# Optimization experiments

Hardware: AMD Instinct MI355X
Metric: run time of the kernel (lower is better)

Reference implementation:

```python
import jax, jax.numpy as jnp
import numpy as np

NUM_FEATURES = 512
NUM_HID = 16
NUM_CLASSES = 40


def _glorot(key, shape):
    lim = float(np.sqrt(6.0 / (shape[0] + shape[1])))
    return jax.random.uniform(key, shape, jnp.float32, -lim, lim)


def setup_inputs() -> dict:
    key = jax.random.key(0)
    k1, k2, k3, k4 = jax.random.split(key, 4)
    N, E = 100000, 3200000
    x = jax.random.normal(k1, (N, NUM_FEATURES), jnp.float32)
    edge_index = jax.random.randint(k2, (2, E), 0, N, jnp.int64)
    W1 = _glorot(k3, (NUM_FEATURES, NUM_HID))
    b1 = jnp.zeros((NUM_HID,), jnp.float32)
    W2 = _glorot(k4, (NUM_HID, NUM_CLASSES))
    b2 = jnp.zeros((NUM_CLASSES,), jnp.float32)
    return {"x": x, "edge_index": edge_index, "num_nodes": N,
            "W1": W1, "b1": b1, "W2": W2, "b2": b2}


def gcn_conv(x, src, dst, norm, W, b, num_nodes):
    # linear transform first (PyG GCNConv), then normalized scatter-add
    h = x @ W                                    # [N, out]
    msg = h[src] * norm[:, None]                 # [E+N, out]
    agg = jax.ops.segment_sum(msg, dst, num_segments=num_nodes)
    return agg + b


def reference(x, edge_index, num_nodes, W1, b1, W2, b2):
    # add self-loops and compute symmetric normalization deg^-1/2 A_hat deg^-1/2
    loops = jnp.arange(num_nodes, dtype=edge_index.dtype)
    src = jnp.concatenate([edge_index[0], loops])
    dst = jnp.concatenate([edge_index[1], loops])
    ones = jnp.ones(src.shape, x.dtype)
    deg = jax.ops.segment_sum(ones, dst, num_segments=num_nodes)
    dinv = jnp.where(deg > 0, deg ** -0.5, 0.0)
    norm = dinv[src] * dinv[dst]

    h = jax.nn.relu(gcn_conv(x, src, dst, norm, W1, b1, num_nodes))
    # dropout omitted: inference mode (training=False)
    h = gcn_conv(h, src, dst, norm, W2, b2, num_nodes)
    out = jax.nn.softmax(h, axis=1)
    return (out, h)
```

## Files before the change

kernel.cpp:

```cpp
#include <hip/hip_runtime.h>
#include <math.h>

#define F 512
#define H 16
#define C 40
#define BW 128
#define BSH 7
#define NB_MAX 1024
#define CHUNK 4096
#define SEGS 8
#define SRC_BITS 17
#define SRC_MASK 0x1FFFF
#define SORT_CAP 8192

__global__ __launch_bounds__(256) void k_hist2(const int* __restrict__ dst,
                                               int* __restrict__ M, int E, int NB) {
    __shared__ int hist[NB_MAX];
    int c = blockIdx.x, t = threadIdx.x;
    for (int b = t; b < NB; b += 256) hist[b] = 0;
    __syncthreads();
    int i0 = c * CHUNK, end = min(i0 + CHUNK, E);
    for (int i = i0 + t; i < end; i += 256)
        atomicAdd(&hist[dst[i] >> BSH], 1);
    __syncthreads();
    for (int b = t; b < NB; b += 256) M[(size_t)c * NB + b] = hist[b];
}

__global__ __launch_bounds__(256) void k_csA(const int* __restrict__ M, int* __restrict__ P,
                                             int NB, int NCH, int SEGLEN) {
    int t = blockIdx.x * 256 + threadIdx.x;
    if (t >= SEGS * NB) return;
    int s = t / NB, b = t - s * NB;
    int c0 = s * SEGLEN, c1 = min(c0 + SEGLEN, NCH);
    int sum = 0;
    for (int c = c0; c < c1; c++) sum += M[(size_t)c * NB + b];
    P[s * NB + b] = sum;
}

__global__ void k_csBscan(int* __restrict__ P, int* __restrict__ brow,
                          int* __restrict__ rowptr, int NB, int N, int E) {
    __shared__ int sh[1024];
    int t = threadIdx.x;
    int run = 0;
    if (t < NB) {
        #pragma unroll
        for (int s = 0; s < SEGS; s++) {
            int v = P[s * NB + t];
            P[s * NB + t] = run;
            run += v;
        }
    }
    sh[t] = run;
    __syncthreads();
    for (int off = 1; off < 1024; off <<= 1) {
        int add = (t >= off) ? sh[t - off] : 0;
        __syncthreads();
        sh[t] += add;
        __syncthreads();
    }
    if (t < NB) brow[t] = sh[t] - run;
    if (t == 0) { brow[NB] = E; rowptr[N] = E; }
}

__global__ __launch_bounds__(256) void k_csC(int* __restrict__ M, const int* __restrict__ P,
                                             const int* __restrict__ brow,
                                             int NB, int NCH, int SEGLEN) {
    int t = blockIdx.x * 256 + threadIdx.x;
    if (t >= SEGS * NB) return;
    int s = t / NB, b = t - s * NB;
    int c0 = s * SEGLEN, c1 = min(c0 + SEGLEN, NCH);
    int run = P[s * NB + b] + brow[b];
    for (int c = c0; c < c1; c++) {
        int v = M[(size_t)c * NB + b];
        M[(size_t)c * NB + b] = run;
        run += v;
    }
}

__global__ __launch_bounds__(256) void k_bscatter3(const int* __restrict__ src,
                                                   const int* __restrict__ dst,
                                                   const int* __restrict__ M,
                                                   int* __restrict__ ebuf, int E, int NB) {
    __shared__ int gbase[NB_MAX];
    __shared__ int pos[NB_MAX];
    __shared__ int cur[NB_MAX];
    __shared__ int tsum[256];
    __shared__ int paddr[CHUNK];
    __shared__ int pdata[CHUNK];
    int c = blockIdx.x, t = threadIdx.x;
    for (int b = t; b < NB; b += 256) {
        gbase[b] = M[(size_t)c * NB + b];
        cur[b] = 0;
    }
    __syncthreads();
    int i0 = c * CHUNK, end = min(i0 + CHUNK, E);
    for (int i = i0 + t; i < end; i += 256)
        atomicAdd(&cur[dst[i] >> BSH], 1);
    __syncthreads();
    int b0 = t * 4;
    int v0 = (b0 + 0 < NB) ? cur[b0 + 0] : 0;
    int v1 = (b0 + 1 < NB) ? cur[b0 + 1] : 0;
    int v2 = (b0 + 2 < NB) ? cur[b0 + 2] : 0;
    int v3 = (b0 + 3 < NB) ? cur[b0 + 3] : 0;
    int loc1 = v0, loc2 = v0 + v1, loc3 = v0 + v1 + v2;
    int s = loc3 + v3;
    tsum[t] = s;
    __syncthreads();
    for (int off = 1; off < 256; off <<= 1) {
        int v = (t >= off) ? tsum[t - off] : 0;
        __syncthreads();
        tsum[t] += v;
        __syncthreads();
    }
    int excl = tsum[t] - s;
    if (b0 + 0 < NB) { int p = excl;        pos[b0 + 0] = p; cur[b0 + 0] = p; }
    if (b0 + 1 < NB) { int p = excl + loc1; pos[b0 + 1] = p; cur[b0 + 1] = p; }
    if (b0 + 2 < NB) { int p = excl + loc2; pos[b0 + 2] = p; cur[b0 + 2] = p; }
    if (b0 + 3 < NB) { int p = excl + loc3; pos[b0 + 3] = p; cur[b0 + 3] = p; }
    __syncthreads();
    for (int i = i0 + t; i < end; i += 256) {
        int d = dst[i], sv = src[i];
        int b = d >> BSH;
        int r = atomicAdd(&cur[b], 1);
        paddr[r] = gbase[b] + (r - pos[b]);
        pdata[r] = ((d & (BW - 1)) << SRC_BITS) | sv;
    }
    __syncthreads();
    int n = end - i0;
    for (int i = t; i < n; i += 256)
        ebuf[paddr[i]] = pdata[i];
}

__global__ __launch_bounds__(256) void k_sortb(int* __restrict__ ebuf,
                                               const int* __restrict__ brow,
                                               int* __restrict__ rowptr,
                                               float* __restrict__ dinv, int N) {
    __shared__ int buf[SORT_CAP];
    __shared__ int hist[BW];
    __shared__ int off[BW];
    __shared__ int cur[BW];
    int b = blockIdx.x;
    int beg = brow[b], end = brow[b + 1];
    int len = end - beg;
    if (len > SORT_CAP) len = SORT_CAP;
    int tid = threadIdx.x;
    if (tid < BW) hist[tid] = 0;
    for (int i = tid; i < len; i += 256) buf[i] = ebuf[beg + i];
    __syncthreads();
    for (int i = tid; i < len; i += 256)
        atomicAdd(&hist[buf[i] >> SRC_BITS], 1);
    __syncthreads();
    if (tid < BW) off[tid] = hist[tid];
    __syncthreads();
    for (int d = 1; d < BW; d <<= 1) {
        int v = (tid < BW && tid >= d) ? off[tid - d] : 0;
        __syncthreads();
        if (tid < BW) off[tid] += v;
        __syncthreads();
    }
    if (tid < BW) {
        int excl = off[tid] - hist[tid];
        int n = b * BW + tid;
        if (n < N) {
            rowptr[n] = beg + excl;
            dinv[n] = rsqrtf((float)(hist[tid] + 1));
        }
        cur[tid] = excl;
    }
    __syncthreads();
    for (int i = tid; i < len; i += 256) {
        int w = buf[i];
        int r = atomicAdd(&cur[w >> SRC_BITS], 1);
        ebuf[beg + r] = w & SRC_MASK;
    }
}

#define KT 64
#define GST 68
__global__ __launch_bounds__(64) void k_gemm1(const float* __restrict__ x,
                                              const float* __restrict__ W1,
                                              const float* __restrict__ dinv,
                                              float* __restrict__ h0s, int N) {
    __shared__ float xs[64 * GST];
    int t = threadIdx.x;
    int n0 = blockIdx.x * 64;
    float acc[H];
    #pragma unroll
    for (int j = 0; j < H; j++) acc[j] = 0.f;
    for (int kt = 0; kt < F; kt += KT) {
        __syncthreads();
        #pragma unroll
        for (int p = 0; p < 16; p++) {
            int idx = t + (p << 6);
            int r = idx >> 4, c4 = idx & 15;
            int v = n0 + r; if (v >= N) v = N - 1;
            float4 val = *(const float4*)(x + (size_t)v * F + kt + (c4 << 2));
            *(float4*)&xs[r * GST + (c4 << 2)] = val;
        }
        __syncthreads();
        #pragma unroll
        for (int k4 = 0; k4 < 16; k4++) {
            float4 xv = *(const float4*)&xs[t * GST + (k4 << 2)];
            const float* w = W1 + (size_t)(kt + (k4 << 2)) * H;
            #pragma unroll
            for (int j = 0; j < H; j++) acc[j] = fmaf(xv.x, w[j], acc[j]);
            #pragma unroll
            for (int j = 0; j < H; j++) acc[j] = fmaf(xv.y, w[H + j], acc[j]);
            #pragma unroll
            for (int j = 0; j < H; j++) acc[j] = fmaf(xv.z, w[2 * H + j], acc[j]);
            #pragma unroll
            for (int j = 0; j < H; j++) acc[j] = fmaf(xv.w, w[3 * H + j], acc[j]);
        }
    }
    int v = n0 + t;
    if (v >= N) return;
    float dv = dinv[v];
    float4* o4 = (float4*)(h0s + (size_t)v * H);
    o4[0] = make_float4(acc[0] * dv, acc[1] * dv, acc[2] * dv, acc[3] * dv);
    o4[1] = make_float4(acc[4] * dv, acc[5] * dv, acc[6] * dv, acc[7] * dv);
    o4[2] = make_float4(acc[8] * dv, acc[9] * dv, acc[10] * dv, acc[11] * dv);
    o4[3] = make_float4(acc[12] * dv, acc[13] * dv, acc[14] * dv, acc[15] * dv);
}

__global__ __launch_bounds__(256) void k_agg1(const float* __restrict__ hs,
                                              const int* __restrict__ adj,
                                              const int* __restrict__ rowptr,
                                              const float* __restrict__ dinv,
                                              const float* __restrict__ b1,
                                              float* __restrict__ out, int N) {
    int t = blockIdx.x * 256 + threadIdx.x;
    int n = t >> 2, q = t & 3;
    if (n >= N) return;
    const float4* hs4 = (const float4*)hs;
    int beg = rowptr[n], end = rowptr[n + 1];
    float4 a = hs4[(size_t)n * 4 + q];
    float ax = a.x, ay = a.y, az = a.z, aw = a.w;
    int e = beg;
    for (; e + 7 < end; e += 8) {
        int s0 = adj[e], s1 = adj[e + 1], s2 = adj[e + 2], s3 = adj[e + 3];
        int s4 = adj[e + 4], s5 = adj[e + 5], s6 = adj[e + 6], s7 = adj[e + 7];
        float4 v0 = hs4[(size_t)s0 * 4 + q];
        float4 v1 = hs4[(size_t)s1 * 4 + q];
        float4 v2 = hs4[(size_t)s2 * 4 + q];
        float4 v3 = hs4[(size_t)s3 * 4 + q];
        float4 v4 = hs4[(size_t)s4 * 4 + q];
        float4 v5 = hs4[(size_t)s5 * 4 + q];
        float4 v6 = hs4[(size_t)s6 * 4 + q];
        float4 v7 = hs4[(size_t)s7 * 4 + q];
        ax += ((v0.x + v1.x) + (v2.x + v3.x)) + ((v4.x + v5.x) + (v6.x + v7.x));
        ay += ((v0.y + v1.y) + (v2.y + v3.y)) + ((v4.y + v5.y) + (v6.y + v7.y));
        az += ((v0.z + v1.z) + (v2.z + v3.z)) + ((v4.z + v5.z) + (v6.z + v7.z));
        aw += ((v0.w + v1.w) + (v2.w + v3.w)) + ((v4.w + v5.w) + (v6.w + v7.w));
    }
    for (; e + 3 < end; e += 4) {
        int s0 = adj[e], s1 = adj[e + 1], s2 = adj[e + 2], s3 = adj[e + 3];
        float4 v0 = hs4[(size_t)s0 * 4 + q];
        float4 v1 = hs4[(size_t)s1 * 4 + q];
        float4 v2 = hs4[(size_t)s2 * 4 + q];
        float4 v3 = hs4[(size_t)s3 * 4 + q];
        ax += (v0.x + v1.x) + (v2.x + v3.x);
        ay += (v0.y + v1.y) + (v2.y + v3.y);
        az += (v0.z + v1.z) + (v2.z + v3.z);
        aw += (v0.w + v1.w) + (v2.w + v3.w);
    }
    for (; e < end; e++) {
        int s = adj[e];
        float4 v = hs4[(size_t)s * 4 + q];
        ax += v.x; ay += v.y; az += v.z; aw += v.w;
    }
    float dv = dinv[n];
    float4 r;
    r.x = fmaxf(fmaf(dv, ax, b1[q * 4 + 0]), 0.f) * dv;
    r.y = fmaxf(fmaf(dv, ay, b1[q * 4 + 1]), 0.f) * dv;
    r.z = fmaxf(fmaf(dv, az, b1[q * 4 + 2]), 0.f) * dv;
    r.w = fmaxf(fmaf(dv, aw, b1[q * 4 + 3]), 0.f) * dv;
    ((float4*)out)[(size_t)n * 4 + q] = r;
}

__global__ __launch_bounds__(256) void k_agg2out(const float* __restrict__ hs,
                                                 const int* __restrict__ adj,
                                                 const int* __restrict__ rowptr,
                                                 const float* __restrict__ dinv,
                                                 const float* __restrict__ W2,
                                                 const float* __restrict__ b2,
                                                 float* __restrict__ dout, int N) {
    __shared__ float sg[64 * 16];
    __shared__ float w2s[H * C];
    __shared__ float b2s[C];
    __shared__ float so[64 * 40];
    int t = threadIdx.x;
    for (int i = t; i < H * C; i += 256) w2s[i] = W2[i];
    if (t < C) b2s[t] = b2[t];
    int nl = t >> 2, q = t & 3;
    int n0 = blockIdx.x * 64;
    int n = n0 + nl;
    bool valid = (n < N);
    int nn = valid ? n : N - 1;
    const float4* hs4 = (const float4*)hs;
    int beg = rowptr[nn], end = rowptr[nn + 1];
    float4 a = hs4[(size_t)nn * 4 + q];
    float ax = a.x, ay = a.y, az = a.z, aw = a.w;
    int e = beg;
    for (; e + 7 < end; e += 8) {
        int s0 = adj[e], s1 = adj[e + 1], s2 = adj[e + 2], s3 = adj[e + 3];
        int s4 = adj[e + 4], s5 = adj[e + 5], s6 = adj[e + 6], s7 = adj[e + 7];
        float4 v0 = hs4[(size_t)s0 * 4 + q];
        float4 v1 = hs4[(size_t)s1 * 4 + q];
        float4 v2 = hs4[(size_t)s2 * 4 + q];
        float4 v3 = hs4[(size_t)s3 * 4 + q];
        float4 v4 = hs4[(size_t)s4 * 4 + q];
        float4 v5 = hs4[(size_t)s5 * 4 + q];
        float4 v6 = hs4[(size_t)s6 * 4 + q];
        float4 v7 = hs4[(size_t)s7 * 4 + q];
        ax += ((v0.x + v1.x) + (v2.x + v3.x)) + ((v4.x + v5.x) + (v6.x + v7.x));
        ay += ((v0.y + v1.y) + (v2.y + v3.y)) + ((v4.y + v5.y) + (v6.y + v7.y));
        az += ((v0.z + v1.z) + (v2.z + v3.z)) + ((v4.z + v5.z) + (v6.z + v7.z));
        aw += ((v0.w + v1.w) + (v2.w + v3.w)) + ((v4.w + v5.w) + (v6.w + v7.w));
    }
    for (; e + 3 < end; e += 4) {
        int s0 = adj[e], s1 = adj[e + 1], s2 = adj[e + 2], s3 = adj[e + 3];
        float4 v0 = hs4[(size_t)s0 * 4 + q];
        float4 v1 = hs4[(size_t)s1 * 4 + q];
        float4 v2 = hs4[(size_t)s2 * 4 + q];
        float4 v3 = hs4[(size_t)s3 * 4 + q];
        ax += (v0.x + v1.x) + (v2.x + v3.x);
        ay += (v0.y + v1.y) + (v2.y + v3.y);
        az += (v0.z + v1.z) + (v2.z + v3.z);
        aw += (v0.w + v1.w) + (v2.w + v3.w);
    }
    for (; e < end; e++) {
        int s = adj[e];
        float4 v = hs4[(size_t)s * 4 + q];
        ax += v.x; ay += v.y; az += v.z; aw += v.w;
    }
    float dv = dinv[nn];
    *(float4*)&sg[nl * 16 + q * 4] = make_float4(dv * ax, dv * ay, dv * az, dv * aw);
    __syncthreads();
    float g16[16];
    #pragma unroll
    for (int k4 = 0; k4 < 4; k4++) {
        float4 gv = *(const float4*)&sg[nl * 16 + k4 * 4];
        g16[k4 * 4] = gv.x; g16[k4 * 4 + 1] = gv.y;
        g16[k4 * 4 + 2] = gv.z; g16[k4 * 4 + 3] = gv.w;
    }
    int j0 = q * 10;
    float h2[10];
    #pragma unroll
    for (int jj = 0; jj < 10; jj++) {
        float acc = b2s[j0 + jj];
        #pragma unroll
        for (int k = 0; k < H; k++) acc = fmaf(g16[k], w2s[k * C + j0 + jj], acc);
        h2[jj] = acc;
    }
    float m = h2[0];
    #pragma unroll
    for (int jj = 1; jj < 10; jj++) m = fmaxf(m, h2[jj]);
    m = fmaxf(m, __shfl_xor(m, 1, 64));
    m = fmaxf(m, __shfl_xor(m, 2, 64));
    float ex[10], ssum = 0.f;
    #pragma unroll
    for (int jj = 0; jj < 10; jj++) { ex[jj] = __expf(h2[jj] - m); ssum += ex[jj]; }
    ssum += __shfl_xor(ssum, 1, 64);
    ssum += __shfl_xor(ssum, 2, 64);
    float inv = 1.f / ssum;
    int rows = min(64, N - n0);
    int tot = rows * 10;
    #pragma unroll
    for (int jj = 0; jj < 10; jj++) so[nl * 40 + j0 + jj] = ex[jj] * inv;
    __syncthreads();
    {
        const float4* sp4 = (const float4*)so;
        float4* o4 = (float4*)(dout + (size_t)n0 * C);
        for (int i = t; i < tot; i += 256) o4[i] = sp4[i];
    }
    __syncthreads();
    #pragma unroll
    for (int jj = 0; jj < 10; jj++) so[nl * 40 + j0 + jj] = h2[jj];
    __syncthreads();
    {
        const float4* sp4 = (const float4*)so;
        float4* o4 = (float4*)(dout + (size_t)N * C + (size_t)n0 * C);
        for (int i = t; i < tot; i += 256) o4[i] = sp4[i];
    }
}

extern "C" void kernel_launch(void* const* d_in, const int* in_sizes, int n_in,
                              void* d_out, int out_size, void* d_ws, size_t ws_size,
                              hipStream_t stream) {
    const float* x  = (const float*)d_in[0];
    const int*   ei = (const int*)d_in[1];
    const float* W1 = (const float*)d_in[3];
    const float* b1 = (const float*)d_in[4];
    const float* W2 = (const float*)d_in[5];
    const float* b2 = (const float*)d_in[6];
    float* out = (float*)d_out;

    int N = in_sizes[0] / F;
    int E = in_sizes[1] / 2;
    const int* src = ei;
    const int* dst = ei + E;
    int NB  = (N + BW - 1) / BW;
    int NCH = (E + CHUNK - 1) / CHUNK;
    int SEGLEN = (NCH + SEGS - 1) / SEGS;

    float* ws = (float*)d_ws;
    size_t o = 0;
    int* M      = (int*)(ws + o); o += (size_t)NCH * NB;
    int* P      = (int*)(ws + o); o += (size_t)SEGS * NB_MAX;
    int* brow   = (int*)(ws + o); o += (size_t)NB_MAX + 4;
    int* rowptr = (int*)(ws + o); o += (size_t)N + 4;
    int* ebuf   = (int*)(ws + o); o += (size_t)E;
    float* dinv = ws + o;         o += (size_t)N;
    float* h0s  = ws + o;         o += (size_t)N * H;
    float* h1s  = ws + o;         o += (size_t)N * H;

    int ng  = (N + 63) / 64;
    int ncs = (SEGS * NB + 255) / 256;

    k_hist2    <<<NCH, 256, 0, stream>>>(dst, M, E, NB);
    k_csA      <<<ncs, 256, 0, stream>>>(M, P, NB, NCH, SEGLEN);
    k_csBscan  <<<1, 1024, 0, stream>>>(P, brow, rowptr, NB, N, E);
    k_csC      <<<ncs, 256, 0, stream>>>(M, P, brow, NB, NCH, SEGLEN);
    k_bscatter3<<<NCH, 256, 0, stream>>>(src, dst, M, ebuf, E, NB);
    k_sortb    <<<NB, 256, 0, stream>>>(ebuf, brow, rowptr, dinv, N);
    k_gemm1    <<<ng, 64, 0, stream>>>(x, W1, dinv, h0s, N);
    k_agg1     <<<(N * 4 + 255) / 256, 256, 0, stream>>>(h0s, ebuf, rowptr, dinv, b1, h1s, N);
    k_agg2out  <<<ng, 256, 0, stream>>>(h1s, ebuf, rowptr, dinv, W2, b2, out, N);
}
```

Baseline: 554.8 us.

## Replace counting-sort prefix pipeline with atomic bucket reservation into fixed-capacity slots

Drops the histogram kernel and the three-kernel column scan over the chunk-by-bucket count matrix. Each chunk now claims space in fixed-stride per-bucket regions (SORT_CAP each) with one global atomicAdd per bucket, and keeps its edges in registers so dst and src are read once. Rows are then addressed by separate begin and end arrays instead of a contiguous rowptr. The cost is a padded edge buffer that makes the adjacency non-contiguous, an extra rowend array, and silent truncation of any bucket holding more than SORT_CAP edges.

```diff
diff --git a/kernel.cpp b/kernel.cpp
--- a/kernel.cpp
+++ b/kernel.cpp
@@ -8,100 +8,42 @@
 #define BSH 7
 #define NB_MAX 1024
 #define CHUNK 4096
-#define SEGS 8
+#define EPT 16
 #define SRC_BITS 17
 #define SRC_MASK 0x1FFFF
 #define SORT_CAP 8192
 
-__global__ __launch_bounds__(256) void k_hist2(const int* __restrict__ dst,
-                                               int* __restrict__ M, int E, int NB) {
+__global__ __launch_bounds__(256) void k_scatfuse(const int* __restrict__ src,
+                                                  const int* __restrict__ dst,
+                                                  int* __restrict__ gcnt,
+                                                  int* __restrict__ ebuf, int E, int NB) {
     __shared__ int hist[NB_MAX];
-    int c = blockIdx.x, t = threadIdx.x;
-    for (int b = t; b < NB; b += 256) hist[b] = 0;
-    __syncthreads();
-    int i0 = c * CHUNK, end = min(i0 + CHUNK, E);
-    for (int i = i0 + t; i < end; i += 256)
-        atomicAdd(&hist[dst[i] >> BSH], 1);
-    __syncthreads();
-    for (int b = t; b < NB; b += 256) M[(size_t)c * NB + b] = hist[b];
-}
-
-__global__ __launch_bounds__(256) void k_csA(const int* __restrict__ M, int* __restrict__ P,
-                                             int NB, int NCH, int SEGLEN) {
-    int t = blockIdx.x * 256 + threadIdx.x;
-    if (t >= SEGS * NB) return;
-    int s = t / NB, b = t - s * NB;
-    int c0 = s * SEGLEN, c1 = min(c0 + SEGLEN, NCH);
-    int sum = 0;
-    for (int c = c0; c < c1; c++) sum += M[(size_t)c * NB + b];
-    P[s * NB + b] = sum;
-}
-
-__global__ void k_csBscan(int* __restrict__ P, int* __restrict__ brow,
-                          int* __restrict__ rowptr, int NB, int N, int E) {
-    __shared__ int sh[1024];
-    int t = threadIdx.x;
-    int run = 0;
-    if (t < NB) {
-        #pragma unroll
-        for (int s = 0; s < SEGS; s++) {
-            int v = P[s * NB + t];
-            P[s * NB + t] = run;
-            run += v;
-        }
-    }
-    sh[t] = run;
-    __syncthreads();
-    for (int off = 1; off < 1024; off <<= 1) {
-        int add = (t >= off) ? sh[t - off] : 0;
-        __syncthreads();
-        sh[t] += add;
-        __syncthreads();
-    }
-    if (t < NB) brow[t] = sh[t] - run;
-    if (t == 0) { brow[NB] = E; rowptr[N] = E; }
-}
-
-__global__ __launch_bounds__(256) void k_csC(int* __restrict__ M, const int* __restrict__ P,
-                                             const int* __restrict__ brow,
-                                             int NB, int NCH, int SEGLEN) {
-    int t = blockIdx.x * 256 + threadIdx.x;
-    if (t >= SEGS * NB) return;
-    int s = t / NB, b = t - s * NB;
-    int c0 = s * SEGLEN, c1 = min(c0 + SEGLEN, NCH);
-    int run = P[s * NB + b] + brow[b];
-    for (int c = c0; c < c1; c++) {
-        int v = M[(size_t)c * NB + b];
-        M[(size_t)c * NB + b] = run;
-        run += v;
-    }
-}
-
-__global__ __launch_bounds__(256) void k_bscatter3(const int* __restrict__ src,
-                                                   const int* __restrict__ dst,
-                                                   const int* __restrict__ M,
-                                                   int* __restrict__ ebuf, int E, int NB) {
-    __shared__ int gbase[NB_MAX];
-    __shared__ int pos[NB_MAX];
+    __shared__ int base2[NB_MAX];
     __shared__ int cur[NB_MAX];
     __shared__ int tsum[256];
     __shared__ int paddr[CHUNK];
     __shared__ int pdata[CHUNK];
     int c = blockIdx.x, t = threadIdx.x;
-    for (int b = t; b < NB; b += 256) {
-        gbase[b] = M[(size_t)c * NB + b];
-        cur[b] = 0;
-    }
-    __syncthreads();
-    int i0 = c * CHUNK, end = min(i0 + CHUNK, E);
-    for (int i = i0 + t; i < end; i += 256)
-        atomicAdd(&cur[dst[i] >> BSH], 1);
+    int i0 = c * CHUNK;
+    int nval = min(CHUNK, E - i0);
+    for (int b = t; b < NB; b += 256) hist[b] = 0;
+    int dreg[EPT], sreg[EPT];
+    #pragma unroll
+    for (int j = 0; j < EPT; j++) {
+        int i = t + j * 256;
+        if (i < nval) { dreg[j] = dst[i0 + i]; sreg[j] = src[i0 + i]; }
+        else dreg[j] = -1;
+    }
+    __syncthreads();
+    #pragma unroll
+    for (int j = 0; j < EPT; j++)
+        if (dreg[j] >= 0) atomicAdd(&hist[dreg[j] >> BSH], 1);
     __syncthreads();
     int b0 = t * 4;
-    int v0 = (b0 + 0 < NB) ? cur[b0 + 0] : 0;
-    int v1 = (b0 + 1 < NB) ? cur[b0 + 1] : 0;
-    int v2 = (b0 + 2 < NB) ? cur[b0 + 2] : 0;
-    int v3 = (b0 + 3 < NB) ? cur[b0 + 3] : 0;
+    int v0 = (b0 + 0 < NB) ? hist[b0 + 0] : 0;
+    int v1 = (b0 + 1 < NB) ? hist[b0 + 1] : 0;
+    int v2 = (b0 + 2 < NB) ? hist[b0 + 2] : 0;
+    int v3 = (b0 + 3 < NB) ? hist[b0 + 3] : 0;
     int loc1 = v0, loc2 = v0 + v1, loc3 = v0 + v1 + v2;
     int s = loc3 + v3;
     tsum[t] = s;
@@ -113,35 +55,37 @@
         __syncthreads();
     }
     int excl = tsum[t] - s;
-    if (b0 + 0 < NB) { int p = excl;        pos[b0 + 0] = p; cur[b0 + 0] = p; }
-    if (b0 + 1 < NB) { int p = excl + loc1; pos[b0 + 1] = p; cur[b0 + 1] = p; }
-    if (b0 + 2 < NB) { int p = excl + loc2; pos[b0 + 2] = p; cur[b0 + 2] = p; }
-    if (b0 + 3 < NB) { int p = excl + loc3; pos[b0 + 3] = p; cur[b0 + 3] = p; }
-    __syncthreads();
-    for (int i = i0 + t; i < end; i += 256) {
-        int d = dst[i], sv = src[i];
+    if (b0 + 0 < NB) { int p = excl;        cur[b0+0] = p; int g = v0 ? atomicAdd(&gcnt[b0+0], v0) : 0; base2[b0+0] = (b0+0)*SORT_CAP + g - p; }
+    if (b0 + 1 < NB) { int p = excl + loc1; cur[b0+1] = p; int g = v1 ? atomicAdd(&gcnt[b0+1], v1) : 0; base2[b0+1] = (b0+1)*SORT_CAP + g - p; }
+    if (b0 + 2 < NB) { int p = excl + loc2; cur[b0+2] = p; int g = v2 ? atomicAdd(&gcnt[b0+2], v2) : 0; base2[b0+2] = (b0+2)*SORT_CAP + g - p; }
+    if (b0 + 3 < NB) { int p = excl + loc3; cur[b0+3] = p; int g = v3 ? atomicAdd(&gcnt[b0+3], v3) : 0; base2[b0+3] = (b0+3)*SORT_CAP + g - p; }
+    __syncthreads();
+    #pragma unroll
+    for (int j = 0; j < EPT; j++) {
+        int d = dreg[j];
+        if (d < 0) continue;
         int b = d >> BSH;
         int r = atomicAdd(&cur[b], 1);
-        paddr[r] = gbase[b] + (r - pos[b]);
-        pdata[r] = ((d & (BW - 1)) << SRC_BITS) | sv;
-    }
-    __syncthreads();
-    int n = end - i0;
-    for (int i = t; i < n; i += 256)
+        paddr[r] = base2[b] + r;
+        pdata[r] = ((d & (BW - 1)) << SRC_BITS) | sreg[j];
+    }
+    __syncthreads();
+    for (int i = t; i < nval; i += 256)
         ebuf[paddr[i]] = pdata[i];
 }
 
 __global__ __launch_bounds__(256) void k_sortb(int* __restrict__ ebuf,
-                                               const int* __restrict__ brow,
-                                               int* __restrict__ rowptr,
+                                               const int* __restrict__ gcnt,
+                                               int* __restrict__ rowbeg,
+                                               int* __restrict__ rowend,
                                                float* __restrict__ dinv, int N) {
     __shared__ int buf[SORT_CAP];
     __shared__ int hist[BW];
     __shared__ int off[BW];
     __shared__ int cur[BW];
     int b = blockIdx.x;
-    int beg = brow[b], end = brow[b + 1];
-    int len = end - beg;
+    int beg = b * SORT_CAP;
+    int len = gcnt[b];
     if (len > SORT_CAP) len = SORT_CAP;
     int tid = threadIdx.x;
     if (tid < BW) hist[tid] = 0;
@@ -162,7 +106,8 @@
         int excl = off[tid] - hist[tid];
         int n = b * BW + tid;
         if (n < N) {
-            rowptr[n] = beg + excl;
+            rowbeg[n] = beg + excl;
+            rowend[n] = beg + off[tid];
             dinv[n] = rsqrtf((float)(hist[tid] + 1));
         }
         cur[tid] = excl;
@@ -224,7 +169,8 @@
 
 __global__ __launch_bounds__(256) void k_agg1(const float* __restrict__ hs,
                                               const int* __restrict__ adj,
-                                              const int* __restrict__ rowptr,
+                                              const int* __restrict__ rowbeg,
+                                              const int* __restrict__ rowend,
                                               const float* __restrict__ dinv,
                                               const float* __restrict__ b1,
                                               float* __restrict__ out, int N) {
@@ -232,7 +178,7 @@
     int n = t >> 2, q = t & 3;
     if (n >= N) return;
     const float4* hs4 = (const float4*)hs;
-    int beg = rowptr[n], end = rowptr[n + 1];
+    int beg = rowbeg[n], end = rowend[n];
     float4 a = hs4[(size_t)n * 4 + q];
     float ax = a.x, ay = a.y, az = a.z, aw = a.w;
     int e = beg;
@@ -279,7 +225,8 @@
 
 __global__ __launch_bounds__(256) void k_agg2out(const float* __restrict__ hs,
                                                  const int* __restrict__ adj,
-                                                 const int* __restrict__ rowptr,
+                                                 const int* __restrict__ rowbeg,
+                                                 const int* __restrict__ rowend,
                                                  const float* __restrict__ dinv,
                                                  const float* __restrict__ W2,
                                                  const float* __restrict__ b2,
@@ -297,7 +244,7 @@
     bool valid = (n < N);
     int nn = valid ? n : N - 1;
     const float4* hs4 = (const float4*)hs;
-    int beg = rowptr[nn], end = rowptr[nn + 1];
+    int beg = rowbeg[nn], end = rowend[nn];
     float4 a = hs4[(size_t)nn * 4 + q];
     float ax = a.x, ay = a.y, az = a.z, aw = a.w;
     int e = beg;
@@ -401,29 +348,23 @@
     const int* dst = ei + E;
     int NB  = (N + BW - 1) / BW;
     int NCH = (E + CHUNK - 1) / CHUNK;
-    int SEGLEN = (NCH + SEGS - 1) / SEGS;
 
     float* ws = (float*)d_ws;
     size_t o = 0;
-    int* M      = (int*)(ws + o); o += (size_t)NCH * NB;
-    int* P      = (int*)(ws + o); o += (size_t)SEGS * NB_MAX;
-    int* brow   = (int*)(ws + o); o += (size_t)NB_MAX + 4;
-    int* rowptr = (int*)(ws + o); o += (size_t)N + 4;
-    int* ebuf   = (int*)(ws + o); o += (size_t)E;
+    int* gcnt   = (int*)(ws + o); o += (size_t)NB_MAX;
+    int* rowbeg = (int*)(ws + o); o += (size_t)N + 4;
+    int* rowend = (int*)(ws + o); o += (size_t)N + 4;
+    int* ebuf   = (int*)(ws + o); o += (size_t)NB * SORT_CAP + CHUNK;
     float* dinv = ws + o;         o += (size_t)N;
     float* h0s  = ws + o;         o += (size_t)N * H;
     float* h1s  = ws + o;         o += (size_t)N * H;
 
-    int ng  = (N + 63) / 64;
-    int ncs = (SEGS * NB + 255) / 256;
-
-    k_hist2    <<<NCH, 256, 0, stream>>>(dst, M, E, NB);
-    k_csA      <<<ncs, 256, 0, stream>>>(M, P, NB, NCH, SEGLEN);
-    k_csBscan  <<<1, 1024, 0, stream>>>(P, brow, rowptr, NB, N, E);
-    k_csC      <<<ncs, 256, 0, stream>>>(M, P, brow, NB, NCH, SEGLEN);
-    k_bscatter3<<<NCH, 256, 0, stream>>>(src, dst, M, ebuf, E, NB);
-    k_sortb    <<<NB, 256, 0, stream>>>(ebuf, brow, rowptr, dinv, N);
-    k_gemm1    <<<ng, 64, 0, stream>>>(x, W1, dinv, h0s, N);
-    k_agg1     <<<(N * 4 + 255) / 256, 256, 0, stream>>>(h0s, ebuf, rowptr, dinv, b1, h1s, N);
-    k_agg2out  <<<ng, 256, 0, stream>>>(h1s, ebuf, rowptr, dinv, W2, b2, out, N);
-}
+    int ng = (N + 63) / 64;
+
+    hipMemsetAsync(gcnt, 0, (size_t)NB * sizeof(int), stream);
+    k_scatfuse<<<NCH, 256, 0, stream>>>(src, dst, gcnt, ebuf, E, NB);
+    k_sortb   <<<NB, 256, 0, stream>>>(ebuf, gcnt, rowbeg, rowend, dinv, N);
+    k_gemm1   <<<ng, 64, 0, stream>>>(x, W1, dinv, h0s, N);
+    k_agg1    <<<(N * 4 + 255) / 256, 256, 0, stream>>>(h0s, ebuf, rowbeg, rowend, dinv, b1, h1s, N);
+    k_agg2out <<<ng, 256, 0, stream>>>(h1s, ebuf, rowbeg, rowend, dinv, W2, b2, out, N);
+}
```

After: 541.1 us. 1.03x faster.
